# Performance work log

Hardware: AMD Instinct MI355X
Metric: run time of the kernel (lower is better)

Reference implementation:

```python
import jax, jax.numpy as jnp
import numpy as np

N = 50000        # nodes per type (MiRNA=0, Disease=1, LncRNA=2)
E = 500000       # edges per relation
F_IN, HID, OUT = 128, 64, 64
ITEMS, SIZE, T = 4096, 4096, 100
# relation order: MvsD, DvsM, MvsL, LvsM, LvsD, DvsL
SRC = (0, 1, 0, 2, 2, 1)
DST = (1, 0, 2, 0, 1, 2)


def _sage_hetero_layer(h, edges, Wp, bp, Ws, bs, Wn):
    """One HeteroGraphConv(SAGEConv pool, aggregate='sum') layer.
    h: list of 3 [N, Fin] node-feature arrays; edges: [6, 2, E] int."""
    n = h[0].shape[0]
    out = [None, None, None]
    for e in range(6):
        s, d = SRC[e], DST[e]
        pooled = jax.nn.relu(h[s] @ Wp[e] + bp[e])                 # [N, Fin]
        msg = pooled[edges[e, 0]]                                  # [E, Fin] gather at src
        agg = jax.ops.segment_max(msg, edges[e, 1], num_segments=n)
        agg = jnp.where(jnp.isneginf(agg), 0.0, agg)               # DGL: 0 for isolated dst
        o = h[d] @ Ws[e] + bs[e] + agg @ Wn[e]                     # fc_self(+bias) + fc_neigh
        out[d] = o if out[d] is None else out[d] + o
    return out


def setup_inputs() -> dict:
    key = jax.random.key(0)
    ks = jax.random.split(key, 32)
    s = 0.05
    inp = {
        'hM': jax.random.normal(ks[0], (N, F_IN), jnp.float32),
        'hD': jax.random.normal(ks[1], (N, F_IN), jnp.float32),
        'hL': jax.random.normal(ks[2], (N, F_IN), jnp.float32),
        'Wpool1': jax.random.normal(ks[3], (6, F_IN, F_IN), jnp.float32) * s,
        'bpool1': jnp.zeros((6, F_IN), jnp.float32),
        'Wself1': jax.random.normal(ks[4], (6, F_IN, HID), jnp.float32) * s,
        'bself1': jnp.zeros((6, HID), jnp.float32),
        'Wneigh1': jax.random.normal(ks[5], (6, F_IN, HID), jnp.float32) * s,
        'Wpool2': jax.random.normal(ks[6], (6, HID, HID), jnp.float32) * s,
        'bpool2': jnp.zeros((6, HID), jnp.float32),
        'Wself2': jax.random.normal(ks[7], (6, HID, HID), jnp.float32) * s,
        'bself2': jnp.zeros((6, HID), jnp.float32),
        'Wneigh2': jax.random.normal(ks[8], (6, HID, HID), jnp.float32) * s,
        'Wpool3': jax.random.normal(ks[9], (6, HID, HID), jnp.float32) * s,
        'bpool3': jnp.zeros((6, HID), jnp.float32),
        'Wself3': jax.random.normal(ks[10], (6, HID, OUT), jnp.float32) * s,
        'bself3': jnp.zeros((6, OUT), jnp.float32),
        'Wneigh3': jax.random.normal(ks[11], (6, HID, OUT), jnp.float32) * s,
        'Adj': jax.random.uniform(ks[12], (SIZE, ITEMS), jnp.float32),
        'noise': jax.random.normal(ks[13], (N, OUT), jnp.float32),
        'W1': jax.random.normal(ks[14], (ITEMS + OUT, 256), jnp.float32) * s,
        'b1': jnp.zeros((256,), jnp.float32),
        'W2': jax.random.normal(ks[15], (256, 512), jnp.float32) * s,
        'b2': jnp.zeros((512,), jnp.float32),
        'W3': jax.random.normal(ks[16], (512, 1024), jnp.float32) * s,
        'b3': jnp.zeros((1024,), jnp.float32),
        'W4': jax.random.normal(ks[17], (1024, ITEMS), jnp.float32) * s,
        'b4': jnp.zeros((ITEMS,), jnp.float32),
        'edges': jax.random.randint(ks[18], (6, 2, E), 0, N, jnp.int32),
        't': 50,
        'size': SIZE,
        'leftIndex': 0,
    }
    return inp


def reference(hM, hD, hL, Wpool1, bpool1, Wself1, bself1, Wneigh1,
              Wpool2, bpool2, Wself2, bself2, Wneigh2,
              Wpool3, bpool3, Wself3, bself3, Wneigh3,
              Adj, noise, W1, b1, W2, b2, W3, b3, W4, b4,
              edges, t, size, leftIndex):
    h1 = _sage_hetero_layer([hM, hD, hL], edges, Wpool1, bpool1, Wself1, bself1, Wneigh1)
    h2 = _sage_hetero_layer(h1, edges, Wpool2, bpool2, Wself2, bself2, Wneigh2)
    h3 = _sage_hetero_layer(h2, edges, Wpool3, bpool3, Wself3, bself3, Wneigh3)
    mirna = h3[0]                                                  # [N, OUT]
    mirna = mirna / jnp.maximum(jnp.sum(jnp.abs(mirna), axis=1, keepdims=True), 1e-12)
    # diffusion schedule
    betas = jnp.linspace(1e-4, 0.02, T, dtype=jnp.float32)
    alpha_bars = jnp.cumprod(1.0 - betas)
    signal_rates = jnp.sqrt(alpha_bars)
    noise_rates = jnp.sqrt(1.0 - alpha_bars)
    noisy = signal_rates[t] * mirna + noise_rates[t] * noise
    fake = jax.lax.stop_gradient(noisy[leftIndex:leftIndex + size])  # detach + slice
    M = jnp.concatenate([Adj, fake], axis=1)                       # [size, ITEMS+OUT]
    x = jax.nn.relu(M @ W1 + b1)
    x = jax.nn.relu(x @ W2 + b2)
    x = jax.nn.relu(x @ W3 + b3)
    x = jax.nn.sigmoid(x @ W4 + b4)
    return fake, x
```

## Files before the change

kernel.cpp:

```cpp
#include <hip/hip_runtime.h>
#include <hip/hip_bf16.h>

#define NNODE 50000
#define NEDGE 500000
#define SZ    4096
#define NBKT  256
#define BWID  196
#define BCAP  4096
#define RELEB ((size_t)NBKT * BCAP)
#define ZK1   8

typedef __attribute__((ext_vector_type(8))) short bf16x8;
typedef __attribute__((ext_vector_type(4))) float f32x4;

__device__ __forceinline__ float bits2f(unsigned short u) {
    return __uint_as_float(((unsigned)u) << 16);
}
__device__ __forceinline__ unsigned short f2bits(float f) {
    unsigned x = __float_as_uint(f);
    unsigned r = x + 0x7fffu + ((x >> 16) & 1u);
    return (unsigned short)(r >> 16);
}
__device__ __forceinline__ unsigned pk_max_u16(unsigned a, unsigned b) {
    unsigned lo = max(a & 0xffffu, b & 0xffffu);
    unsigned hi = max(a >> 16, b >> 16);
    return lo | (hi << 16);
}
__device__ __forceinline__ void gl_lds16(const void* g, void* l) {
    __builtin_amdgcn_global_load_lds(
        (const __attribute__((address_space(1))) unsigned int*)g,
        (__attribute__((address_space(3))) unsigned int*)l, 16, 0, 0);
}

template<int RELU, int SIG, int OUTF32, int PART>
__global__ __launch_bounds__(256)
void gemm128(const unsigned short* __restrict__ A, const unsigned short* __restrict__ Bt,
             const float* __restrict__ bias, void* __restrict__ Cv, int M, int N, int K)
{
    __shared__ unsigned short As[2][128 * 64];
    __shared__ unsigned short Bs[2][128 * 64];
    const int tid = threadIdx.x;
    const int wave = tid >> 6, lane = tid & 63;
    const int m16 = lane & 15, quad = lane >> 4;
    const int wr = wave >> 1, wc = wave & 1;
    const int nwg = gridDim.x * gridDim.y;
    int bid = blockIdx.y * gridDim.x + blockIdx.x;
    if ((nwg & 7) == 0) { int cpx = nwg >> 3; bid = (bid & 7) * cpx + (bid >> 3); }
    const int bx = bid % gridDim.x, by = bid / gridDim.x;
    const int row0 = by * 128, col0 = bx * 128;
    const int lrow = lane >> 3, lcol = (lane & 7) * 8;

    f32x4 acc[4][4] = {};

    int k0beg = 0, k0end = K;
    if (PART) {
        const int per = ((K >> 6) + gridDim.z - 1) / gridDim.z;
        k0beg = blockIdx.z * per * 64;
        k0end = min(K, k0beg + per * 64);
    }
    const int nt = (k0end - k0beg) >> 6;

    auto STAGE = [&](int b, int k0) {
#pragma unroll
        for (int i = 0; i < 4; ++i) {
            int chunk = wave * 4 + i;
            int row = chunk * 8 + lrow;
            gl_lds16(A  + (size_t)(row0 + row) * K + k0 + lcol, &As[b][chunk * 512]);
            gl_lds16(Bt + (size_t)(col0 + row) * K + k0 + lcol, &Bs[b][chunk * 512]);
        }
    };

    STAGE(0, k0beg);
    __syncthreads();
    int cur = 0;
    for (int t = 0; t < nt; ++t) {
        if (t + 1 < nt) STAGE(cur ^ 1, k0beg + (t + 1) * 64);
#pragma unroll
        for (int ks = 0; ks < 2; ++ks) {
            bf16x8 a[4], b[4];
#pragma unroll
            for (int mt = 0; mt < 4; ++mt)
                a[mt] = *(const bf16x8*)&As[cur][(wr * 64 + mt * 16 + m16) * 64 + ks * 32 + quad * 8];
#pragma unroll
            for (int nt2 = 0; nt2 < 4; ++nt2)
                b[nt2] = *(const bf16x8*)&Bs[cur][(wc * 64 + nt2 * 16 + m16) * 64 + ks * 32 + quad * 8];
#pragma unroll
            for (int mt = 0; mt < 4; ++mt)
#pragma unroll
                for (int nt2 = 0; nt2 < 4; ++nt2)
                    acc[mt][nt2] = __builtin_amdgcn_mfma_f32_16x16x32_bf16(a[mt], b[nt2], acc[mt][nt2], 0, 0, 0);
        }
        __syncthreads();
        cur ^= 1;
    }

    if (PART) {
        float* P = (float*)Cv + (size_t)blockIdx.z * M * N;
#pragma unroll
        for (int mt = 0; mt < 4; ++mt)
#pragma unroll
            for (int nt2 = 0; nt2 < 4; ++nt2) {
                int gc = col0 + wc * 64 + nt2 * 16 + m16;
#pragma unroll
                for (int r = 0; r < 4; ++r) {
                    int gm = row0 + wr * 64 + mt * 16 + quad * 4 + r;
                    P[(size_t)gm * N + gc] = acc[mt][nt2][r];
                }
            }
        return;
    }

#pragma unroll
    for (int mt = 0; mt < 4; ++mt) {
#pragma unroll
        for (int nt2 = 0; nt2 < 4; ++nt2) {
            int gc = col0 + wc * 64 + nt2 * 16 + m16;
            float bv = bias[gc];
#pragma unroll
            for (int r = 0; r < 4; ++r) {
                int gm = row0 + wr * 64 + mt * 16 + quad * 4 + r;
                size_t idx = (size_t)gm * N + gc;
                float v = acc[mt][nt2][r] + bv;
                if (RELU) v = fmaxf(v, 0.f);
                if (SIG)  v = 1.f / (1.f + __expf(-v));
                if (OUTF32) ((float*)Cv)[idx] = v;
                else        ((unsigned short*)Cv)[idx] = f2bits(v);
            }
        }
    }
}

__global__ __launch_bounds__(256)
void mlp1_ep_k(const float* __restrict__ p, const float* __restrict__ b1,
               unsigned short* __restrict__ x1)
{
    const size_t MN = (size_t)SZ * 256;
    int i = blockIdx.x * 256 + threadIdx.x;
    if (i >= (int)(MN / 4)) return;
    float4 s = ((const float4*)p)[i];
#pragma unroll
    for (int z = 1; z < ZK1; ++z) {
        float4 a = ((const float4*)(p + (size_t)z * MN))[i];
        s.x += a.x; s.y += a.y; s.z += a.z; s.w += a.w;
    }
    int base = i * 4;
    ushort4 o;
    o.x = f2bits(fmaxf(s.x + b1[(base + 0) & 255], 0.f));
    o.y = f2bits(fmaxf(s.y + b1[(base + 1) & 255], 0.f));
    o.z = f2bits(fmaxf(s.z + b1[(base + 2) & 255], 0.f));
    o.w = f2bits(fmaxf(s.w + b1[(base + 3) & 255], 0.f));
    ((ushort4*)x1)[i] = o;
}

template<int NT>
__global__ __launch_bounds__(256)
void pool2_k(const unsigned short* __restrict__ A0, const unsigned short* __restrict__ A1,
             const unsigned short* __restrict__ Bt0, const unsigned short* __restrict__ Bt1,
             const float* __restrict__ b0, const float* __restrict__ b1,
             unsigned short* __restrict__ out, int M, int K)
{
    __shared__ unsigned short As[64][72];
    __shared__ unsigned short Bs[NT * 16][72];
    const int z = blockIdx.z;
    const unsigned short* A = z ? A1 : A0;
    const unsigned short* Bt = z ? Bt1 : Bt0;
    const float* bias = z ? b1 : b0;
    const int N = NT * 16;
    unsigned short* Cv = out + (size_t)z * M * N;

    const int tid = threadIdx.x;
    const int wave = tid >> 6, lane = tid & 63;
    const int m16 = lane & 15, quad = lane >> 4;
    const int row0 = blockIdx.y * 64, col0 = blockIdx.x * N;

    f32x4 acc[NT] = {};

    for (int k0 = 0; k0 < K; k0 += 64) {
#pragma unroll
        for (int it = 0; it < 2; ++it) {
            int u = tid + it * 256;
            int m = u >> 3, c = (u & 7) * 8;
            int gm = row0 + m;
            uint4 v = make_uint4(0u, 0u, 0u, 0u);
            if (gm < M) v = *(const uint4*)(A + (size_t)gm * K + k0 + c);
            *(uint4*)&As[m][c] = v;
        }
#pragma unroll
        for (int it = 0; it < NT / 2; ++it) {
            int u = tid + it * 256;
            int n = u >> 3, c = (u & 7) * 8;
            uint4 v = *(const uint4*)(Bt + (size_t)(col0 + n) * K + k0 + c);
            *(uint4*)&Bs[n][c] = v;
        }
        __syncthreads();
#pragma unroll
        for (int ks = 0; ks < 2; ++ks) {
            bf16x8 a = *(const bf16x8*)&As[wave * 16 + m16][ks * 32 + quad * 8];
#pragma unroll
            for (int nt = 0; nt < NT; ++nt) {
                bf16x8 b = *(const bf16x8*)&Bs[nt * 16 + m16][ks * 32 + quad * 8];
                acc[nt] = __builtin_amdgcn_mfma_f32_16x16x32_bf16(a, b, acc[nt], 0, 0, 0);
            }
        }
        __syncthreads();
    }

#pragma unroll
    for (int nt = 0; nt < NT; ++nt) {
        int gc = col0 + nt * 16 + m16;
        float bv = bias[gc];
#pragma unroll
        for (int r = 0; r < 4; ++r) {
            int gm = row0 + wave * 16 + quad * 4 + r;
            if (gm < M)
                Cv[(size_t)gm * N + gc] = f2bits(fmaxf(acc[nt][r] + bv, 0.f));
        }
    }
}

__global__ __launch_bounds__(256)
void pool6_k(const unsigned short* __restrict__ hin, const unsigned short* __restrict__ pT,
             const float* __restrict__ bp, unsigned short* __restrict__ pooled6, int M)
{
    const int SRCr[6] = {0, 1, 0, 2, 2, 1};
    __shared__ unsigned short As[64][72];
    __shared__ unsigned short Bs[64][72];
    const int z = blockIdx.z;
    const unsigned short* A = hin + (size_t)SRCr[z] * M * 64;
    const unsigned short* Bt = pT + (size_t)z * 4096;
    const float* bias = bp + z * 64;
    unsigned short* Cv = pooled6 + (size_t)z * M * 64;

    const int tid = threadIdx.x;
    const int wave = tid >> 6, lane = tid & 63;
    const int m16 = lane & 15, quad = lane >> 4;
    const int row0 = blockIdx.y * 64;

    f32x4 acc[4] = {};

    {
#pragma unroll
        for (int it = 0; it < 2; ++it) {
            int u = tid + it * 256;
            int m = u >> 3, c = (u & 7) * 8;
            int gm = row0 + m;
            uint4 v = make_uint4(0u, 0u, 0u, 0u);
            if (gm < M) v = *(const uint4*)(A + (size_t)gm * 64 + c);
            *(uint4*)&As[m][c] = v;
        }
#pragma unroll
        for (int it = 0; it < 2; ++it) {
            int u = tid + it * 256;
            int n = u >> 3, c = (u & 7) * 8;
            uint4 v = *(const uint4*)(Bt + (size_t)n * 64 + c);
            *(uint4*)&Bs[n][c] = v;
        }
        __syncthreads();
#pragma unroll
        for (int ks = 0; ks < 2; ++ks) {
            bf16x8 a = *(const bf16x8*)&As[wave * 16 + m16][ks * 32 + quad * 8];
#pragma unroll
            for (int nt = 0; nt < 4; ++nt) {
                bf16x8 b = *(const bf16x8*)&Bs[nt * 16 + m16][ks * 32 + quad * 8];
                acc[nt] = __builtin_amdgcn_mfma_f32_16x16x32_bf16(a, b, acc[nt], 0, 0, 0);
            }
        }
    }

#pragma unroll
    for (int nt = 0; nt < 4; ++nt) {
        int gc = nt * 16 + m16;
        float bv = bias[gc];
#pragma unroll
        for (int r = 0; r < 4; ++r) {
            int gm = row0 + wave * 16 + quad * 4 + r;
            if (gm < M)
                Cv[(size_t)gm * 64 + gc] = f2bits(fmaxf(acc[nt][r] + bv, 0.f));
        }
    }
}

template<int NT>
__global__ __launch_bounds__(256)
void mfma_gemm(const unsigned short* __restrict__ A1, const unsigned short* __restrict__ A2,
               const unsigned short* __restrict__ A3,
               const unsigned short* __restrict__ Bt, const float* __restrict__ bias,
               const float* __restrict__ bias2,
               unsigned short* __restrict__ Cv, int M, int N, int Ka, int Kb, int Kc)
{
    __shared__ unsigned short As[64][72];
    __shared__ unsigned short Bs[NT * 16][72];
    const int tid = threadIdx.x;
    const int wave = tid >> 6, lane = tid & 63;
    const int m16 = lane & 15, quad = lane >> 4;
    const int row0 = blockIdx.y * 64, col0 = blockIdx.x * (NT * 16);
    const int K = Ka + Kb + Kc;

    f32x4 acc[NT] = {};

    for (int k0 = 0; k0 < K; k0 += 64) {
        const int seg = (k0 >= Ka + Kb) ? 2 : ((k0 >= Ka) ? 1 : 0);
        const unsigned short* src = seg == 2 ? A3 : (seg == 1 ? A2 : A1);
        const int ld = seg == 2 ? Kc : (seg == 1 ? Kb : Ka);
        const int kb = k0 - (seg == 2 ? Ka + Kb : (seg == 1 ? Ka : 0));
#pragma unroll
        for (int it = 0; it < 2; ++it) {
            int u = tid + it * 256;
            int m = u >> 3, c = (u & 7) * 8;
            int gm = row0 + m;
            uint4 v = make_uint4(0u, 0u, 0u, 0u);
            if (gm < M) v = *(const uint4*)(src + (size_t)gm * ld + kb + c);
            *(uint4*)&As[m][c] = v;
        }
#pragma unroll
        for (int it = 0; it < NT / 2; ++it) {
            int u = tid + it * 256;
            int n = u >> 3, c = (u & 7) * 8;
            uint4 v = *(const uint4*)(Bt + (size_t)(col0 + n) * K + k0 + c);
            *(uint4*)&Bs[n][c] = v;
        }
        __syncthreads();
#pragma unroll
        for (int ks = 0; ks < 2; ++ks) {
            bf16x8 a = *(const bf16x8*)&As[wave * 16 + m16][ks * 32 + quad * 8];
#pragma unroll
            for (int nt = 0; nt < NT; ++nt) {
                bf16x8 b = *(const bf16x8*)&Bs[nt * 16 + m16][ks * 32 + quad * 8];
                acc[nt] = __builtin_amdgcn_mfma_f32_16x16x32_bf16(a, b, acc[nt], 0, 0, 0);
            }
        }
        __syncthreads();
    }

#pragma unroll
    for (int nt = 0; nt < NT; ++nt) {
        int gc = col0 + nt * 16 + m16;
        float bv = bias[gc] + bias2[gc];
#pragma unroll
        for (int r = 0; r < 4; ++r) {
            int gm = row0 + wave * 16 + quad * 4 + r;
            if (gm < M)
                Cv[(size_t)gm * N + gc] = f2bits(acc[nt][r] + bv);
        }
    }
}

__global__ __launch_bounds__(256)
void fused3_k(const unsigned short* __restrict__ hin,
              const unsigned short* __restrict__ regA, const unsigned short* __restrict__ regB,
              const unsigned short* __restrict__ fT, const float* __restrict__ bs,
              unsigned short* __restrict__ hout, int M)
{
    const int PAe[3] = {1, 0, 2}, PBe[3] = {3, 4, 5};
    __shared__ unsigned short As[64][72];
    __shared__ unsigned short Bs[64][72];
    const int z = blockIdx.z;
    const int eA = PAe[z], eB = PBe[z];
    const unsigned short* A1 = hin + (size_t)z * M * 64;
    const unsigned short* A2 = (eA < 4) ? regA + (size_t)eA * M * 64 : regB + (size_t)(eA - 4) * M * 64;
    const unsigned short* A3 = (eB < 4) ? regA + (size_t)eB * M * 64 : regB + (size_t)(eB - 4) * M * 64;
    const unsigned short* Bt = fT + (size_t)z * 12288;
    const float* bias = bs + eA * 64;
    const float* bias2 = bs + eB * 64;
    unsigned short* Cv = hout + (size_t)z * M * 64;

    const int tid = threadIdx.x;
    const int wave = tid >> 6, lane = tid & 63;
    const int m16 = lane & 15, quad = lane >> 4;
    const int row0 = blockIdx.y * 64;

    f32x4 acc[4] = {};

#pragma unroll
    for (int seg = 0; seg < 3; ++seg) {
        const unsigned short* src = seg == 2 ? A3 : (seg == 1 ? A2 : A1);
        const int k0 = seg * 64;
#pragma unroll
        for (int it = 0; it < 2; ++it) {
            int u = tid + it * 256;
            int m = u >> 3, c = (u & 7) * 8;
            int gm = row0 + m;
            uint4 v = make_uint4(0u, 0u, 0u, 0u);
            if (gm < M) v = *(const uint4*)(src + (size_t)gm * 64 + c);
            *(uint4*)&As[m][c] = v;
        }
#pragma unroll
        for (int it = 0; it < 2; ++it) {
            int u = tid + it * 256;
            int n = u >> 3, c = (u & 7) * 8;
            uint4 v = *(const uint4*)(Bt + (size_t)n * 192 + k0 + c);
            *(uint4*)&Bs[n][c] = v;
        }
        __syncthreads();
#pragma unroll
        for (int ks = 0; ks < 2; ++ks) {
            bf16x8 a = *(const bf16x8*)&As[wave * 16 + m16][ks * 32 + quad * 8];
#pragma unroll
            for (int nt = 0; nt < 4; ++nt) {
                bf16x8 b = *(const bf16x8*)&Bs[nt * 16 + m16][ks * 32 + quad * 8];
                acc[nt] = __builtin_amdgcn_mfma_f32_16x16x32_bf16(a, b, acc[nt], 0, 0, 0);
            }
        }
        __syncthreads();
    }

#pragma unroll
    for (int nt = 0; nt < 4; ++nt) {
        int gc = nt * 16 + m16;
        float bv = bias[gc] + bias2[gc];
#pragma unroll
        for (int r = 0; r < 4; ++r) {
            int gm = row0 + wave * 16 + quad * 4 + r;
            if (gm < M)
                Cv[(size_t)gm * 64 + gc] = f2bits(acc[nt][r] + bv);
        }
    }
}

__global__ __launch_bounds__(256)
void transpose_cvt(const float* __restrict__ src1, const float* __restrict__ src2,
                   unsigned short* __restrict__ dst, int R1, int R2, int Nn)
{
    __shared__ float tile[32][33];
    const int R = R1 + R2;
    const int e = blockIdx.z;
    src1 += (size_t)e * R1 * Nn;
    if (src2) src2 += (size_t)e * R2 * Nn;
    dst += (size_t)e * Nn * R;
    const int r0 = blockIdx.x * 32, n0 = blockIdx.y * 32;
    const int lr = threadIdx.x >> 5, ln = threadIdx.x & 31;
#pragma unroll
    for (int i = 0; i < 4; ++i) {
        int r = r0 + lr + i * 8, n = n0 + ln;
        float v = 0.f;
        if (r < R && n < Nn) v = (r < R1) ? src1[(size_t)r * Nn + n]
                                          : src2[(size_t)(r - R1) * Nn + n];
        tile[lr + i * 8][ln] = v;
    }
    __syncthreads();
#pragma unroll
    for (int i = 0; i < 4; ++i) {
        int n = n0 + lr + i * 8, r = r0 + ln;
        if (n < Nn && r < R) dst[(size_t)n * R + r] = f2bits(tile[ln][lr + i * 8]);
    }
}

__global__ __launch_bounds__(256)
void fuse_w_k(const float* __restrict__ Ws, const float* __restrict__ Wn,
              unsigned short* __restrict__ dst, int F)
{
    const int PAe[3] = {1, 0, 2}, PBe[3] = {3, 4, 5};
    __shared__ float tile[32][33];
    const int p = blockIdx.z;
    const int eA = PAe[p], eB = PBe[p];
    const int Kt = 3 * F;
    unsigned short* D = dst + (size_t)p * 64 * Kt;
    const int r0 = blockIdx.x * 32;
    const int n0 = blockIdx.y * 32;
    const int lr = threadIdx.x >> 5, ln = threadIdx.x & 31;
    for (int seg = 0; seg < 3; ++seg) {
        __syncthreads();
#pragma unroll
        for (int i = 0; i < 4; ++i) {
            int r = r0 + lr + i * 8, n = n0 + ln;
            float v;
            if (seg == 0)
                v = Ws[((size_t)eA * F + r) * 64 + n] + Ws[((size_t)eB * F + r) * 64 + n];
            else if (seg == 1)
                v = Wn[((size_t)eA * F + r) * 64 + n];
            else
                v = Wn[((size_t)eB * F + r) * 64 + n];
            tile[lr + i * 8][ln] = v;
        }
        __syncthreads();
        const int koff = seg * F;
#pragma unroll
        for (int i = 0; i < 4; ++i) {
            int n = n0 + lr + i * 8, r = r0 + ln;
            D[(size_t)n * Kt + koff + r] = f2bits(tile[ln][lr + i * 8]);
        }
    }
}

__global__ __launch_bounds__(256)
void cvt3_k(const float* __restrict__ s0, const float* __restrict__ s1,
            const float* __restrict__ s2, unsigned short* __restrict__ dst)
{
    const int z = blockIdx.z;
    const float* src = z == 0 ? s0 : (z == 1 ? s1 : s2);
    dst += (size_t)z * NNODE * 128;
    int i = blockIdx.x * 256 + threadIdx.x;
    if (i >= 1600000) return;
    float4 v = ((const float4*)src)[i];
    ushort4 w;
    w.x = f2bits(v.x); w.y = f2bits(v.y); w.z = f2bits(v.z); w.w = f2bits(v.w);
    ((ushort4*)dst)[i] = w;
}

__global__ __launch_bounds__(256)
void cvt_adj_k(const float* __restrict__ src, unsigned short* __restrict__ dst)
{
    int i = blockIdx.x * 256 + threadIdx.x;
    if (i >= 4194304) return;
    int r = i >> 10, c4 = i & 1023;
    float4 v = ((const float4*)src)[i];
    ushort4 w;
    w.x = f2bits(v.x); w.y = f2bits(v.y); w.z = f2bits(v.z); w.w = f2bits(v.w);
    *(ushort4*)(dst + (size_t)r * 4160 + c4 * 4) = w;
}

__global__ __launch_bounds__(256)
void binit_k(int* __restrict__ bcur)
{
    bcur[blockIdx.x * NBKT + threadIdx.x] = threadIdx.x * BCAP;
}

__global__ __launch_bounds__(256)
void bucket_k(const int* __restrict__ edges, int* __restrict__ bcur,
              unsigned* __restrict__ ebuf)
{
    const int r = blockIdx.y;
    const int base = blockIdx.x * 4096;
    const int tid = threadIdx.x;
    __shared__ int lcnt[NBKT];
    __shared__ int lbase[NBKT];
    for (int i = tid; i < NBKT; i += 256) lcnt[i] = 0;
    __syncthreads();
    unsigned ent[16];
    int rnk[16];
#pragma unroll
    for (int i = 0; i < 16; ++i) {
        int e = base + tid + i * 256;
        ent[i] = 0xffffffffu;
        rnk[i] = 0;
        if (e < NEDGE) {
            int src = edges[(size_t)r * 2 * NEDGE + e];
            int dst = edges[(size_t)r * 2 * NEDGE + NEDGE + e];
            ent[i] = ((unsigned)dst << 16) | (unsigned)src;
            rnk[i] = atomicAdd(&lcnt[dst / BWID], 1);
        }
    }
    __syncthreads();
    for (int i = tid; i < NBKT; i += 256)
        lbase[i] = lcnt[i] ? atomicAdd(&bcur[r * NBKT + i], lcnt[i]) : 0;
    __syncthreads();
#pragma unroll
    for (int i = 0; i < 16; ++i)
        if (ent[i] != 0xffffffffu) {
            int b = (int)(ent[i] >> 16) / BWID;
            int pos = lbase[b] + rnk[i];
            if (pos < (b + 1) * BCAP)
                ebuf[(size_t)r * RELEB + pos] = ent[i];
        }
}

__global__ __launch_bounds__(256)
void bscan_k(const int* __restrict__ bcur, int* __restrict__ bbase,
             int* __restrict__ offs)
{
    const int r = blockIdx.x, tid = threadIdx.x;
    const int lane = tid & 63, wv = tid >> 6;
    int v = bcur[r * NBKT + tid] - tid * BCAP;
    if (v > BCAP) v = BCAP;
    int x = v;
#pragma unroll
    for (int off = 1; off < 64; off <<= 1) {
        int t = __shfl_up(x, off);
        if (lane >= off) x += t;
    }
    __shared__ int wsum[4];
    if (lane == 63) wsum[wv] = x;
    __syncthreads();
    int add = 0;
#pragma unroll
    for (int w = 0; w < 4; ++w) if (w < wv) add += wsum[w];
    x += add;
    bbase[r * NBKT + tid] = x - v;
    if (tid == 255) offs[(size_t)r * (NNODE + 1) + NNODE] = x;
}

__global__ __launch_bounds__(256)
void debucket_k(const unsigned* __restrict__ ebuf, const int* __restrict__ bcur,
                const int* __restrict__ bbase, int* __restrict__ offs,
                unsigned short* __restrict__ srcs)
{
    const int r = blockIdx.y, b = blockIdx.x, tid = threadIdx.x;
    const int lo = b * BWID;
    __shared__ unsigned es[BCAP];
    __shared__ unsigned short stage[BCAP];
    __shared__ int lhist[256];
    __shared__ int buf[256];
    __shared__ int lcur[256];
    int cnt = bcur[r * NBKT + b] - b * BCAP;
    if (cnt > BCAP) cnt = BCAP;
    const int base = bbase[r * NBKT + b];
    lhist[tid] = 0;
    __syncthreads();
    for (int j = tid; j < cnt; j += 256) {
        unsigned e = ebuf[(size_t)r * RELEB + (size_t)b * BCAP + j];
        es[j] = e;
        atomicAdd(&lhist[(int)(e >> 16) - lo], 1);
    }
    __syncthreads();
    int v = lhist[tid];
    buf[tid] = v;
    __syncthreads();
    for (int off = 1; off < 256; off <<= 1) {
        int t = (tid >= off) ? buf[tid - off] : 0;
        __syncthreads();
        buf[tid] += t;
        __syncthreads();
    }
    int excl = buf[tid] - v;
    int node = lo + tid;
    if (tid < BWID && node < NNODE) offs[(size_t)r * (NNODE + 1) + node] = base + excl;
    lcur[tid] = excl;
    __syncthreads();
    for (int j = tid; j < cnt; j += 256) {
        unsigned e = es[j];
        int d = (int)(e >> 16) - lo;
        int p = atomicAdd(&lcur[d], 1);
        stage[p] = (unsigned short)(e & 0xffffu);
    }
    __syncthreads();
    for (int j = tid; j < cnt; j += 256)
        srcs[(size_t)r * NEDGE + base + j] = stage[j];
}

template<int F>
__global__ __launch_bounds__(256)
void gather2_k(const unsigned short* __restrict__ pooled, const int* __restrict__ offs,
               const unsigned short* __restrict__ srcs, unsigned short* __restrict__ agg,
               int e0, int e1)
{
    const int CG = F / 8;
    const int z = blockIdx.z;
    const int e = z ? e1 : e0;
    pooled += (size_t)z * NNODE * F;
    agg    += (size_t)z * NNODE * F;
    offs   += (size_t)e * (NNODE + 1);
    srcs   += (size_t)e * NEDGE;
    int idx = blockIdx.x * 256 + threadIdx.x;
    int n = idx / CG, cg = idx % CG;
    if (n >= NNODE) return;
    int beg = offs[n], end = offs[n + 1];
    unsigned m0 = 0, m1 = 0, m2 = 0, m3 = 0;
    int j = beg;
    for (; j + 4 <= end; j += 4) {
        int s0 = srcs[j], s1 = srcs[j + 1], s2 = srcs[j + 2], s3 = srcs[j + 3];
        uint4 v0 = *(const uint4*)(pooled + (size_t)s0 * F + cg * 8);
        uint4 v1 = *(const uint4*)(pooled + (size_t)s1 * F + cg * 8);
        uint4 v2 = *(const uint4*)(pooled + (size_t)s2 * F + cg * 8);
        uint4 v3 = *(const uint4*)(pooled + (size_t)s3 * F + cg * 8);
        m0 = pk_max_u16(m0, pk_max_u16(pk_max_u16(v0.x, v1.x), pk_max_u16(v2.x, v3.x)));
        m1 = pk_max_u16(m1, pk_max_u16(pk_max_u16(v0.y, v1.y), pk_max_u16(v2.y, v3.y)));
        m2 = pk_max_u16(m2, pk_max_u16(pk_max_u16(v0.z, v1.z), pk_max_u16(v2.z, v3.z)));
        m3 = pk_max_u16(m3, pk_max_u16(pk_max_u16(v0.w, v1.w), pk_max_u16(v2.w, v3.w)));
    }
    for (; j < end; ++j) {
        int s = srcs[j];
        uint4 v = *(const uint4*)(pooled + (size_t)s * F + cg * 8);
        m0 = pk_max_u16(m0, v.x);
        m1 = pk_max_u16(m1, v.y);
        m2 = pk_max_u16(m2, v.z);
        m3 = pk_max_u16(m3, v.w);
    }
    uint4 o; o.x = m0; o.y = m1; o.z = m2; o.w = m3;
    *(uint4*)(agg + (size_t)n * F + cg * 8) = o;
}

__global__ __launch_bounds__(256)
void gather6_k(const unsigned short* __restrict__ pooled6, const int* __restrict__ offs,
               const unsigned short* __restrict__ srcs,
               unsigned short* __restrict__ regA, unsigned short* __restrict__ regB)
{
    const int F = 64, CG = 8;
    const int z = blockIdx.z;
    const unsigned short* pooled = pooled6 + (size_t)z * NNODE * F;
    unsigned short* agg = (z < 4) ? regA + (size_t)z * NNODE * F
                                  : regB + (size_t)(z - 4) * NNODE * F;
    offs += (size_t)z * (NNODE + 1);
    srcs += (size_t)z * NEDGE;
    int idx = blockIdx.x * 256 + threadIdx.x;
    int n = idx / CG, cg = idx % CG;
    if (n >= NNODE) return;
    int beg = offs[n], end = offs[n + 1];
    unsigned m0 = 0, m1 = 0, m2 = 0, m3 = 0;
    int j = beg;
    for (; j + 4 <= end; j += 4) {
        int s0 = srcs[j], s1 = srcs[j + 1], s2 = srcs[j + 2], s3 = srcs[j + 3];
        uint4 v0 = *(const uint4*)(pooled + (size_t)s0 * F + cg * 8);
        uint4 v1 = *(const uint4*)(pooled + (size_t)s1 * F + cg * 8);
        uint4 v2 = *(const uint4*)(pooled + (size_t)s2 * F + cg * 8);
        uint4 v3 = *(const uint4*)(pooled + (size_t)s3 * F + cg * 8);
        m0 = pk_max_u16(m0, pk_max_u16(pk_max_u16(v0.x, v1.x), pk_max_u16(v2.x, v3.x)));
        m1 = pk_max_u16(m1, pk_max_u16(pk_max_u16(v0.y, v1.y), pk_max_u16(v2.y, v3.y)));
        m2 = pk_max_u16(m2, pk_max_u16(pk_max_u16(v0.z, v1.z), pk_max_u16(v2.z, v3.z)));
        m3 = pk_max_u16(m3, pk_max_u16(pk_max_u16(v0.w, v1.w), pk_max_u16(v2.w, v3.w)));
    }
    for (; j < end; ++j) {
        int s = srcs[j];
        uint4 v = *(const uint4*)(pooled + (size_t)s * F + cg * 8);
        m0 = pk_max_u16(m0, v.x);
        m1 = pk_max_u16(m1, v.y);
        m2 = pk_max_u16(m2, v.z);
        m3 = pk_max_u16(m3, v.w);
    }
    uint4 o; o.x = m0; o.y = m1; o.z = m2; o.w = m3;
    *(uint4*)(agg + (size_t)n * F + cg * 8) = o;
}

__global__ __launch_bounds__(64)
void fake_k(const unsigned short* __restrict__ mirna, const float* __restrict__ noise,
            const int* __restrict__ t_p, const int* __restrict__ left_p,
            unsigned short* __restrict__ adj_s, float* __restrict__ fake_out)
{
    int r = blockIdx.x, c = threadIdx.x;
    int t = *t_p, left = *left_p;
    int row = left + r;
    float x = bits2f(mirna[(size_t)row * 64 + c]);
    float s = fabsf(x);
#pragma unroll
    for (int off = 32; off > 0; off >>= 1) s += __shfl_down(s, off);
    s = __shfl(s, 0);
    float ab = 1.f;
    for (int i = 0; i <= t; ++i)
        ab *= (1.f - (1e-4f + (0.02f - 1e-4f) * ((float)i / 99.f)));
    float v = sqrtf(ab) * (x / fmaxf(s, 1e-12f)) + sqrtf(1.f - ab) * noise[(size_t)row * 64 + c];
    adj_s[(size_t)r * 4160 + 4096 + c] = f2bits(v);
    fake_out[(size_t)r * 64 + c] = v;
}

extern "C" void kernel_launch(void* const* d_in, const int* in_sizes, int n_in,
                              void* d_out, int out_size, void* d_ws, size_t ws_size,
                              hipStream_t stream)
{
    const float* h0[3]    = {(const float*)d_in[0], (const float*)d_in[1], (const float*)d_in[2]};
    const float* Wpool[3] = {(const float*)d_in[3], (const float*)d_in[8],  (const float*)d_in[13]};
    const float* bpool[3] = {(const float*)d_in[4], (const float*)d_in[9],  (const float*)d_in[14]};
    const float* bself[3] = {(const float*)d_in[6], (const float*)d_in[11], (const float*)d_in[16]};
    const float* Wself[3] = {(const float*)d_in[5], (const float*)d_in[10], (const float*)d_in[15]};
    const float* Wneigh[3]= {(const float*)d_in[7], (const float*)d_in[12], (const float*)d_in[17]};
    const float* Adj   = (const float*)d_in[18];
    const float* noise = (const float*)d_in[19];
    const float* W1 = (const float*)d_in[20]; const float* b1 = (const float*)d_in[21];
    const float* W2 = (const float*)d_in[22]; const float* b2 = (const float*)d_in[23];
    const float* W3 = (const float*)d_in[24]; const float* b3 = (const float*)d_in[25];
    const float* W4 = (const float*)d_in[26]; const float* b4 = (const float*)d_in[27];
    const int* edges  = (const int*)d_in[28];
    const int* t_p    = (const int*)d_in[29];
    const int* left_p = (const int*)d_in[31];

    unsigned short* ws = (unsigned short*)d_ws;
    const size_t P1 = 0, P2 = 98304, P3 = 122880;
    const size_t FU1 = 147456, FU2 = 245760, FU3 = 294912;
    const size_t W1T = 344064, W2T = 1409024, W3T = 1540096, W4T = 2064384;
    const size_t ADJ = 6258688;
    const size_t POOLED = 23298048;
    const size_t HA = 36098048, HB = 45698048;
    int* bcur  = (int*)(ws + 55298048);
    int* bbase = bcur + 6 * NBKT;
    int* offs  = bbase + 6 * NBKT;
    unsigned short* srcs = (unsigned short*)(offs + 6 * (NNODE + 1));
    unsigned* ebuf = (unsigned*)(ws + POOLED);
    unsigned short* x1 = ws + POOLED;
    unsigned short* x2 = x1 + (size_t)SZ * 256;
    unsigned short* x3 = x2 + (size_t)SZ * 512;
    unsigned short* adj_s = ws + ADJ;
    float* out_fake = (float*)d_out;
    float* out_x    = out_fake + (size_t)SZ * 64;
    unsigned short* hb0 = (unsigned short*)out_x;
    unsigned short* agg2_l1 = hb0 + 19200000;
    unsigned short* pooled6 = (unsigned short*)out_x;
    unsigned short* aggB6 = pooled6 + 19200000;
    unsigned short* aggA6 = ws + POOLED;
    float* x1p = out_x;

    const int SRCr[6] = {0, 1, 0, 2, 2, 1};
    const int PAe[3] = {1, 0, 2}, PBe[3] = {3, 4, 5};
    dim3 T(256);

    transpose_cvt<<<dim3(4, 4, 6),   T, 0, stream>>>(Wpool[0], nullptr, ws + P1, 128, 0, 128);
    transpose_cvt<<<dim3(2, 2, 6),   T, 0, stream>>>(Wpool[1], nullptr, ws + P2, 64, 0, 64);
    transpose_cvt<<<dim3(2, 2, 6),   T, 0, stream>>>(Wpool[2], nullptr, ws + P3, 64, 0, 64);
    fuse_w_k<<<dim3(4, 2, 3), T, 0, stream>>>(Wself[0], Wneigh[0], ws + FU1, 128);
    fuse_w_k<<<dim3(2, 2, 3), T, 0, stream>>>(Wself[1], Wneigh[1], ws + FU2, 64);
    fuse_w_k<<<dim3(2, 2, 3), T, 0, stream>>>(Wself[2], Wneigh[2], ws + FU3, 64);
    transpose_cvt<<<dim3(130, 8, 1), T, 0, stream>>>(W1, nullptr, ws + W1T, 4160, 0, 256);
    transpose_cvt<<<dim3(8, 16, 1),  T, 0, stream>>>(W2, nullptr, ws + W2T, 256, 0, 512);
    transpose_cvt<<<dim3(16, 32, 1), T, 0, stream>>>(W3, nullptr, ws + W3T, 512, 0, 1024);
    transpose_cvt<<<dim3(32, 128, 1),T, 0, stream>>>(W4, nullptr, ws + W4T, 1024, 0, 4096);
    cvt_adj_k<<<16384, T, 0, stream>>>(Adj, adj_s);
    cvt3_k<<<dim3(6250, 1, 3), T, 0, stream>>>(h0[0], h0[1], h0[2], hb0);

    binit_k<<<6, T, 0, stream>>>(bcur);
    bucket_k<<<dim3(123, 6), T, 0, stream>>>(edges, bcur, ebuf);
    bscan_k<<<6, T, 0, stream>>>(bcur, bbase, offs);
    debucket_k<<<dim3(NBKT, 6), T, 0, stream>>>(ebuf, bcur, bbase, offs, srcs);

    for (int p = 0; p < 3; ++p) {
        const int eA = PAe[p], eB = PBe[p];
        pool2_k<8><<<dim3(1, 782, 2), T, 0, stream>>>(
            hb0 + (size_t)SRCr[eA] * NNODE * 128, hb0 + (size_t)SRCr[eB] * NNODE * 128,
            ws + P1 + (size_t)eA * 16384, ws + P1 + (size_t)eB * 16384,
            bpool[0] + eA * 128, bpool[0] + eB * 128,
            ws + POOLED, NNODE, 128);
        gather2_k<128><<<dim3(3125, 1, 2), T, 0, stream>>>(
            ws + POOLED, offs, srcs, agg2_l1, eA, eB);
        mfma_gemm<4><<<dim3(1, 782), T, 0, stream>>>(
            hb0 + (size_t)p * NNODE * 128, agg2_l1, agg2_l1 + (size_t)NNODE * 128,
            ws + FU1 + (size_t)p * 24576, bself[0] + eA * 64, bself[0] + eB * 64,
            ws + HA + (size_t)p * NNODE * 64, NNODE, 64, 128, 128, 128);
    }

    unsigned short* hin = ws + HA;
    unsigned short* hout = ws + HB;
    for (int layer = 1; layer <= 2; ++layer) {
        const unsigned short* pT = ws + (layer == 1 ? P2 : P3);
        const unsigned short* fT = ws + (layer == 1 ? FU2 : FU3);
        pool6_k<<<dim3(1, 782, 6), T, 0, stream>>>(hin, pT, bpool[layer], pooled6, NNODE);
        gather6_k<<<dim3(1563, 1, 6), T, 0, stream>>>(pooled6, offs, srcs, aggA6, aggB6);
        fused3_k<<<dim3(1, 782, 3), T, 0, stream>>>(hin, aggA6, aggB6, fT,
                                                    bself[layer], hout, NNODE);
        unsigned short* tmp = hin; hin = hout; hout = tmp;
    }

    fake_k<<<SZ, dim3(64), 0, stream>>>(hin, noise, t_p, left_p, adj_s, out_fake);

    gemm128<0, 0, 0, 1><<<dim3(2, 32, ZK1), T, 0, stream>>>(
        adj_s, ws + W1T, b1, x1p, SZ, 256, 4160);
    mlp1_ep_k<<<1024, T, 0, stream>>>(x1p, b1, x1);
    gemm128<1, 0, 0, 0><<<dim3(4, 32),  T, 0, stream>>>(x1, ws + W2T, b2, x2, SZ, 512, 256);
    gemm128<1, 0, 0, 0><<<dim3(8, 32),  T, 0, stream>>>(x2, ws + W3T, b3, x3, SZ, 1024, 512);
    gemm128<0, 1, 1, 0><<<dim3(32, 32), T, 0, stream>>>(x3, ws + W4T, b4, out_x, SZ, 4096, 1024);
}
```

Measured before the change: 871.7 us.

## Phase gathers by source-node range and single-buffer the final GEMM

The segment-max gather kernels now sweep each destination's edge list several times (4 phases for layer 1, 2 for layers 2-3). Each pass only loads pooled rows whose source index falls in one node range, so the working set of concurrently gathered rows is smaller and more likely to stay in cache. The cost is re-reading the source index list once per phase and adding branch divergence. Separately, the last 4096x4096 GEMM switches to a single LDS buffer with no prefetch, halving its shared memory to allow more resident blocks at the cost of losing load/compute overlap.

```diff
diff --git a/kernel.cpp b/kernel.cpp
--- a/kernel.cpp
+++ b/kernel.cpp
@@ -32,13 +32,13 @@
         (__attribute__((address_space(3))) unsigned int*)l, 16, 0, 0);
 }
 
-template<int RELU, int SIG, int OUTF32, int PART>
+template<int RELU, int SIG, int OUTF32, int PART, int PIPE>
 __global__ __launch_bounds__(256)
 void gemm128(const unsigned short* __restrict__ A, const unsigned short* __restrict__ Bt,
              const float* __restrict__ bias, void* __restrict__ Cv, int M, int N, int K)
 {
-    __shared__ unsigned short As[2][128 * 64];
-    __shared__ unsigned short Bs[2][128 * 64];
+    __shared__ unsigned short As[PIPE + 1][128 * 64];
+    __shared__ unsigned short Bs[PIPE + 1][128 * 64];
     const int tid = threadIdx.x;
     const int wave = tid >> 6, lane = tid & 63;
     const int m16 = lane & 15, quad = lane >> 4;
@@ -69,29 +69,41 @@
             gl_lds16(Bt + (size_t)(col0 + row) * K + k0 + lcol, &Bs[b][chunk * 512]);
         }
     };
-
-    STAGE(0, k0beg);
-    __syncthreads();
-    int cur = 0;
-    for (int t = 0; t < nt; ++t) {
-        if (t + 1 < nt) STAGE(cur ^ 1, k0beg + (t + 1) * 64);
+    auto COMPUTE = [&](int b) {
 #pragma unroll
         for (int ks = 0; ks < 2; ++ks) {
-            bf16x8 a[4], b[4];
+            bf16x8 a[4], bb[4];
 #pragma unroll
             for (int mt = 0; mt < 4; ++mt)
-                a[mt] = *(const bf16x8*)&As[cur][(wr * 64 + mt * 16 + m16) * 64 + ks * 32 + quad * 8];
+                a[mt] = *(const bf16x8*)&As[b][(wr * 64 + mt * 16 + m16) * 64 + ks * 32 + quad * 8];
 #pragma unroll
             for (int nt2 = 0; nt2 < 4; ++nt2)
-                b[nt2] = *(const bf16x8*)&Bs[cur][(wc * 64 + nt2 * 16 + m16) * 64 + ks * 32 + quad * 8];
+                bb[nt2] = *(const bf16x8*)&Bs[b][(wc * 64 + nt2 * 16 + m16) * 64 + ks * 32 + quad * 8];
 #pragma unroll
             for (int mt = 0; mt < 4; ++mt)
 #pragma unroll
                 for (int nt2 = 0; nt2 < 4; ++nt2)
-                    acc[mt][nt2] = __builtin_amdgcn_mfma_f32_16x16x32_bf16(a[mt], b[nt2], acc[mt][nt2], 0, 0, 0);
-        }
-        __syncthreads();
-        cur ^= 1;
+                    acc[mt][nt2] = __builtin_amdgcn_mfma_f32_16x16x32_bf16(a[mt], bb[nt2], acc[mt][nt2], 0, 0, 0);
+        }
+    };
+
+    if (PIPE) {
+        STAGE(0, k0beg);
+        __syncthreads();
+        int cur = 0;
+        for (int t = 0; t < nt; ++t) {
+            if (t + 1 < nt) STAGE(cur ^ 1, k0beg + (t + 1) * 64);
+            COMPUTE(cur);
+            __syncthreads();
+            cur ^= 1;
+        }
+    } else {
+        for (int t = 0; t < nt; ++t) {
+            STAGE(0, k0beg + t * 64);
+            __syncthreads();
+            COMPUTE(0);
+            __syncthreads();
+        }
     }
 
     if (PART) {
@@ -627,46 +639,70 @@
         srcs[(size_t)r * NEDGE + base + j] = stage[j];
 }
 
-template<int F>
-__global__ __launch_bounds__(256)
-void gather2_k(const unsigned short* __restrict__ pooled, const int* __restrict__ offs,
-               const unsigned short* __restrict__ srcs, unsigned short* __restrict__ agg,
-               int e0, int e1)
+template<int F, int PH>
+__device__ __forceinline__ void gather_body(
+    const unsigned short* __restrict__ pooled, const int* __restrict__ offs,
+    const unsigned short* __restrict__ srcs, unsigned short* __restrict__ agg)
 {
     const int CG = F / 8;
-    const int z = blockIdx.z;
-    const int e = z ? e1 : e0;
-    pooled += (size_t)z * NNODE * F;
-    agg    += (size_t)z * NNODE * F;
-    offs   += (size_t)e * (NNODE + 1);
-    srcs   += (size_t)e * NEDGE;
     int idx = blockIdx.x * 256 + threadIdx.x;
     int n = idx / CG, cg = idx % CG;
     if (n >= NNODE) return;
     int beg = offs[n], end = offs[n + 1];
     unsigned m0 = 0, m1 = 0, m2 = 0, m3 = 0;
-    int j = beg;
-    for (; j + 4 <= end; j += 4) {
-        int s0 = srcs[j], s1 = srcs[j + 1], s2 = srcs[j + 2], s3 = srcs[j + 3];
-        uint4 v0 = *(const uint4*)(pooled + (size_t)s0 * F + cg * 8);
-        uint4 v1 = *(const uint4*)(pooled + (size_t)s1 * F + cg * 8);
-        uint4 v2 = *(const uint4*)(pooled + (size_t)s2 * F + cg * 8);
-        uint4 v3 = *(const uint4*)(pooled + (size_t)s3 * F + cg * 8);
-        m0 = pk_max_u16(m0, pk_max_u16(pk_max_u16(v0.x, v1.x), pk_max_u16(v2.x, v3.x)));
-        m1 = pk_max_u16(m1, pk_max_u16(pk_max_u16(v0.y, v1.y), pk_max_u16(v2.y, v3.y)));
-        m2 = pk_max_u16(m2, pk_max_u16(pk_max_u16(v0.z, v1.z), pk_max_u16(v2.z, v3.z)));
-        m3 = pk_max_u16(m3, pk_max_u16(pk_max_u16(v0.w, v1.w), pk_max_u16(v2.w, v3.w)));
-    }
-    for (; j < end; ++j) {
-        int s = srcs[j];
-        uint4 v = *(const uint4*)(pooled + (size_t)s * F + cg * 8);
-        m0 = pk_max_u16(m0, v.x);
-        m1 = pk_max_u16(m1, v.y);
-        m2 = pk_max_u16(m2, v.z);
-        m3 = pk_max_u16(m3, v.w);
+    const int step = (NNODE + PH - 1) / PH;
+#pragma unroll 1
+    for (int ph = 0; ph < PH; ++ph) {
+        const int plo = ph * step, phi = plo + step;
+        int j = beg;
+        for (; j + 4 <= end; j += 4) {
+            int s0 = srcs[j], s1 = srcs[j + 1], s2 = srcs[j + 2], s3 = srcs[j + 3];
+            if (s0 >= plo && s0 < phi) {
+                uint4 v = *(const uint4*)(pooled + (size_t)s0 * F + cg * 8);
+                m0 = pk_max_u16(m0, v.x); m1 = pk_max_u16(m1, v.y);
+                m2 = pk_max_u16(m2, v.z); m3 = pk_max_u16(m3, v.w);
+            }
+            if (s1 >= plo && s1 < phi) {
+                uint4 v = *(const uint4*)(pooled + (size_t)s1 * F + cg * 8);
+                m0 = pk_max_u16(m0, v.x); m1 = pk_max_u16(m1, v.y);
+                m2 = pk_max_u16(m2, v.z); m3 = pk_max_u16(m3, v.w);
+            }
+            if (s2 >= plo && s2 < phi) {
+                uint4 v = *(const uint4*)(pooled + (size_t)s2 * F + cg * 8);
+                m0 = pk_max_u16(m0, v.x); m1 = pk_max_u16(m1, v.y);
+                m2 = pk_max_u16(m2, v.z); m3 = pk_max_u16(m3, v.w);
+            }
+            if (s3 >= plo && s3 < phi) {
+                uint4 v = *(const uint4*)(pooled + (size_t)s3 * F + cg * 8);
+                m0 = pk_max_u16(m0, v.x); m1 = pk_max_u16(m1, v.y);
+                m2 = pk_max_u16(m2, v.z); m3 = pk_max_u16(m3, v.w);
+            }
+        }
+        for (; j < end; ++j) {
+            int s = srcs[j];
+            if (s >= plo && s < phi) {
+                uint4 v = *(const uint4*)(pooled + (size_t)s * F + cg * 8);
+                m0 = pk_max_u16(m0, v.x); m1 = pk_max_u16(m1, v.y);
+                m2 = pk_max_u16(m2, v.z); m3 = pk_max_u16(m3, v.w);
+            }
+        }
     }
     uint4 o; o.x = m0; o.y = m1; o.z = m2; o.w = m3;
     *(uint4*)(agg + (size_t)n * F + cg * 8) = o;
+}
+
+template<int F>
+__global__ __launch_bounds__(256)
+void gather2_k(const unsigned short* __restrict__ pooled, const int* __restrict__ offs,
+               const unsigned short* __restrict__ srcs, unsigned short* __restrict__ agg,
+               int e0, int e1)
+{
+    const int z = blockIdx.z;
+    const int e = z ? e1 : e0;
+    gather_body<F, 4>(pooled + (size_t)z * NNODE * F,
+                      offs + (size_t)e * (NNODE + 1),
+                      srcs + (size_t)e * NEDGE,
+                      agg + (size_t)z * NNODE * F);
 }
 
 __global__ __launch_bounds__(256)
@@ -674,40 +710,14 @@
                const unsigned short* __restrict__ srcs,
                unsigned short* __restrict__ regA, unsigned short* __restrict__ regB)
 {
-    const int F = 64, CG = 8;
+    const int F = 64;
     const int z = blockIdx.z;
-    const unsigned short* pooled = pooled6 + (size_t)z * NNODE * F;
     unsigned short* agg = (z < 4) ? regA + (size_t)z * NNODE * F
                                   : regB + (size_t)(z - 4) * NNODE * F;
-    offs += (size_t)z * (NNODE + 1);
-    srcs += (size_t)z * NEDGE;
-    int idx = blockIdx.x * 256 + threadIdx.x;
-    int n = idx / CG, cg = idx % CG;
-    if (n >= NNODE) return;
-    int beg = offs[n], end = offs[n + 1];
-    unsigned m0 = 0, m1 = 0, m2 = 0, m3 = 0;
-    int j = beg;
-    for (; j + 4 <= end; j += 4) {
-        int s0 = srcs[j], s1 = srcs[j + 1], s2 = srcs[j + 2], s3 = srcs[j + 3];
-        uint4 v0 = *(const uint4*)(pooled + (size_t)s0 * F + cg * 8);
-        uint4 v1 = *(const uint4*)(pooled + (size_t)s1 * F + cg * 8);
-        uint4 v2 = *(const uint4*)(pooled + (size_t)s2 * F + cg * 8);
-        uint4 v3 = *(const uint4*)(pooled + (size_t)s3 * F + cg * 8);
-        m0 = pk_max_u16(m0, pk_max_u16(pk_max_u16(v0.x, v1.x), pk_max_u16(v2.x, v3.x)));
-        m1 = pk_max_u16(m1, pk_max_u16(pk_max_u16(v0.y, v1.y), pk_max_u16(v2.y, v3.y)));
-        m2 = pk_max_u16(m2, pk_max_u16(pk_max_u16(v0.z, v1.z), pk_max_u16(v2.z, v3.z)));
-        m3 = pk_max_u16(m3, pk_max_u16(pk_max_u16(v0.w, v1.w), pk_max_u16(v2.w, v3.w)));
-    }
-    for (; j < end; ++j) {
-        int s = srcs[j];
-        uint4 v = *(const uint4*)(pooled + (size_t)s * F + cg * 8);
-        m0 = pk_max_u16(m0, v.x);
-        m1 = pk_max_u16(m1, v.y);
-        m2 = pk_max_u16(m2, v.z);
-        m3 = pk_max_u16(m3, v.w);
-    }
-    uint4 o; o.x = m0; o.y = m1; o.z = m2; o.w = m3;
-    *(uint4*)(agg + (size_t)n * F + cg * 8) = o;
+    gather_body<F, 2>(pooled6 + (size_t)z * NNODE * F,
+                      offs + (size_t)z * (NNODE + 1),
+                      srcs + (size_t)z * NEDGE,
+                      agg);
 }
 
 __global__ __launch_bounds__(64)
@@ -827,10 +837,10 @@
 
     fake_k<<<SZ, dim3(64), 0, stream>>>(hin, noise, t_p, left_p, adj_s, out_fake);
 
-    gemm128<0, 0, 0, 1><<<dim3(2, 32, ZK1), T, 0, stream>>>(
+    gemm128<0, 0, 0, 1, 1><<<dim3(2, 32, ZK1), T, 0, stream>>>(
         adj_s, ws + W1T, b1, x1p, SZ, 256, 4160);
     mlp1_ep_k<<<1024, T, 0, stream>>>(x1p, b1, x1);
-    gemm128<1, 0, 0, 0><<<dim3(4, 32),  T, 0, stream>>>(x1, ws + W2T, b2, x2, SZ, 512, 256);
-    gemm128<1, 0, 0, 0><<<dim3(8, 32),  T, 0, stream>>>(x2, ws + W3T, b3, x3, SZ, 1024, 512);
-    gemm128<0, 1, 1, 0><<<dim3(32, 32), T, 0, stream>>>(x3, ws + W4T, b4, out_x, SZ, 4096, 1024);
-}
+    gemm128<1, 0, 0, 0, 1><<<dim3(4, 32),  T, 0, stream>>>(x1, ws + W2T, b2, x2, SZ, 512, 256);
+    gemm128<1, 0, 0, 0, 1><<<dim3(8, 32),  T, 0, stream>>>(x2, ws + W3T, b3, x3, SZ, 1024, 512);
+    gemm128<0, 1, 1, 0, 0><<<dim3(32, 32), T, 0, stream>>>(x3, ws + W4T, b4, out_x, SZ, 4096, 1024);
+}
```

Result: slower. 1.088 ms (+24.8%).
